# Optimization experiments

Hardware: AMD Instinct MI355X
Metric: run time of the kernel (lower is better)

Reference implementation:

```python
import jax, jax.numpy as jnp
import numpy as np
import math

D_MODEL = 1024
N_HEAD = 16
D_K = D_MODEL // N_HEAD
B, S = 2, 2048


def setup_inputs() -> dict:
    key = jax.random.key(0)
    ks = jax.random.split(key, 9)
    sc = 0.02
    return {
        "x": jax.random.normal(ks[0], (B, S, D_MODEL), dtype=jnp.float32),
        "Wq": jax.random.normal(ks[1], (D_MODEL, D_MODEL), dtype=jnp.float32) * sc,
        "bq": jnp.zeros((D_MODEL,), dtype=jnp.float32),
        "Wk": jax.random.normal(ks[2], (D_MODEL, D_MODEL), dtype=jnp.float32) * sc,
        "bk": jnp.zeros((D_MODEL,), dtype=jnp.float32),
        "Wv": jax.random.normal(ks[3], (D_MODEL, D_MODEL), dtype=jnp.float32) * sc,
        "bv": jnp.zeros((D_MODEL,), dtype=jnp.float32),
        "Wo": jax.random.normal(ks[4], (D_MODEL, D_MODEL), dtype=jnp.float32) * sc,
        "bo": jnp.zeros((D_MODEL,), dtype=jnp.float32),
    }


def reference(x, Wq, bq, Wk, bk, Wv, bv, Wo, bo):
    # cache=None prefill path: q_start=0, k_len=S (S <= MAX_CACHE_LEN)
    b, s, d = x.shape
    # projections (torch Linear: x @ W.T + b)
    q = (x @ Wq.T + bq).reshape(b, s, N_HEAD, D_K).transpose(0, 2, 1, 3)  # [b,h,s,dk]
    k = (x @ Wk.T + bk).reshape(b, s, N_HEAD, D_K).transpose(0, 2, 1, 3)
    v = (x @ Wv.T + bv).reshape(b, s, N_HEAD, D_K).transpose(0, 2, 1, 3)
    scores = jnp.einsum("bhqd,bhkd->bhqk", q, k) / math.sqrt(D_K)
    causal = jnp.triu(jnp.ones((s, s), dtype=bool), k=1)  # True above diagonal
    scores = jnp.where(causal[None, None], -jnp.inf, scores)
    attn = jax.nn.softmax(scores, axis=-1)  # dropout p=0 (eval)
    ctx = jnp.einsum("bhqk,bhkd->bhqd", attn, v)
    ctx = ctx.transpose(0, 2, 1, 3).reshape(b, s, d)
    return ctx @ Wo.T + bo
```

## Files before the change

### kernel.cpp

```cpp
#include <hip/hip_runtime.h>
#include <hip/hip_bf16.h>

#define DM 1024
#define NH 16
#define DK 64
#define BB 2
#define SS 2048
#define NTOK (BB*SS)
#define SCALE_LOG2E 0.1803368801111204f

typedef __attribute__((ext_vector_type(8))) short bf16x8;
typedef __attribute__((ext_vector_type(4))) float f32x4;
typedef __attribute__((ext_vector_type(4))) unsigned short us4;
typedef __attribute__((ext_vector_type(4))) unsigned int u32x4;

#define GLOAD16(gp, lp) \
  __builtin_amdgcn_global_load_lds((const __attribute__((address_space(1))) void*)(gp), \
                                   (__attribute__((address_space(3))) void*)(lp), 16, 0, 0)

__device__ inline unsigned short f2b(float f) {
  unsigned int x = __float_as_uint(f);
  return (unsigned short)((x + 0x7FFFu + ((x >> 16) & 1u)) >> 16);
}
__device__ inline unsigned int pack2bf(float a, float b) {
  unsigned int r;
  asm("v_cvt_pk_bf16_f32 %0, %1, %2" : "=v"(r) : "v"(a), "v"(b));
  return r;
}

#define XC4 (NTOK*DM/4)
#define WC4 (DM*DM/4)
__global__ void cast_all(const float* __restrict__ x,  const float* __restrict__ wq,
                         const float* __restrict__ wk, const float* __restrict__ wv,
                         const float* __restrict__ wo,
                         unsigned short* __restrict__ xb,  unsigned short* __restrict__ wqb,
                         unsigned short* __restrict__ wkb, unsigned short* __restrict__ wvb,
                         unsigned short* __restrict__ wob) {
  const int total = XC4 + 4*WC4;
  int i = blockIdx.x * blockDim.x + threadIdx.x;
  int stride = gridDim.x * blockDim.x;
  for (; i < total; i += stride) {
    const float* s; unsigned short* d; int off;
    if (i < XC4) { s = x; d = xb; off = i; }
    else {
      int j = i - XC4;
      int sel = j >> 18;
      off = j & (WC4 - 1);
      if      (sel == 0) { s = wq; d = wqb; }
      else if (sel == 1) { s = wk; d = wkb; }
      else if (sel == 2) { s = wv; d = wvb; }
      else               { s = wo; d = wob; }
    }
    float4 v = reinterpret_cast<const float4*>(s)[off];
    us4 o;
    o[0] = f2b(v.x); o[1] = f2b(v.y); o[2] = f2b(v.z); o[3] = f2b(v.w);
    reinterpret_cast<us4*>(d)[off] = o;
  }
}

__device__ __forceinline__ void gemm_mainloop(const unsigned short* __restrict__ A,
                                              const unsigned short* __restrict__ W,
                                              unsigned short* As, unsigned short* Bs,
                                              int m0, int n0, int tid, f32x4 acc[4][2]) {
  const int lane = tid & 63;
  const int w = tid >> 6;
  const int wr = w >> 1, wc = w & 1;
  const int g = lane >> 4, q = lane & 15;

  const int col0 = (((lane & 7) ^ ((lane >> 3) & 7)) << 3);
  const unsigned short* Ag = A + (size_t)(m0 + w*32 + (lane >> 3)) * DM + col0;
  const unsigned short* Bg = W + (size_t)(n0 + w*16 + (lane >> 3)) * DM + col0;
  char* AsB = (char*)As + w * 4096;
  char* BsB = (char*)Bs + w * 2048;

  const int fso = ((g ^ (q & 7)) << 4);

  for (int kt = 0; kt < DM; kt += 64) {
    __syncthreads();
    GLOAD16(Ag + kt,          AsB);
    GLOAD16(Ag + kt +  8*DM,  AsB + 1024);
    GLOAD16(Ag + kt + 16*DM,  AsB + 2048);
    GLOAD16(Ag + kt + 24*DM,  AsB + 3072);
    GLOAD16(Bg + kt,          BsB);
    GLOAD16(Bg + kt +  8*DM,  BsB + 1024);
    __syncthreads();
    #pragma unroll
    for (int h = 0; h < 2; h++) {
      const int so = fso ^ (h << 6);
      bf16x8 aF[4], bF[2];
      #pragma unroll
      for (int mt = 0; mt < 4; mt++)
        aF[mt] = *reinterpret_cast<const bf16x8*>((char*)As + (wr*64 + mt*16 + q)*128 + so);
      #pragma unroll
      for (int nt = 0; nt < 2; nt++)
        bF[nt] = *reinterpret_cast<const bf16x8*>((char*)Bs + (wc*32 + nt*16 + q)*128 + so);
      #pragma unroll
      for (int mt = 0; mt < 4; mt++)
        #pragma unroll
        for (int nt = 0; nt < 2; nt++)
          acc[mt][nt] = __builtin_amdgcn_mfma_f32_16x16x32_bf16(aF[mt], bF[nt], acc[mt][nt], 0, 0, 0);
    }
  }
}

__global__ __launch_bounds__(256, 2)
void gemm_qkv(const unsigned short* __restrict__ xb,
              const unsigned short* __restrict__ wqb, const unsigned short* __restrict__ wkb,
              const unsigned short* __restrict__ wvb,
              const float* __restrict__ bq, const float* __restrict__ bk,
              const float* __restrict__ bv,
              unsigned short* __restrict__ qo, unsigned short* __restrict__ ko,
              unsigned short* __restrict__ vto) {
  __shared__ unsigned short As[128*64];
  __shared__ unsigned short Bs[64*64];
  const int z = blockIdx.z;
  const unsigned short* W = (z == 0) ? wqb : (z == 1) ? wkb : wvb;
  const float* bias = (z == 0) ? bq : (z == 1) ? bk : bv;
  const int m0 = blockIdx.y * 128, n0 = blockIdx.x * 64;

  f32x4 acc[4][2];
  #pragma unroll
  for (int i = 0; i < 4; i++)
    #pragma unroll
    for (int j = 0; j < 2; j++)
      #pragma unroll
      for (int e = 0; e < 4; e++) acc[i][j][e] = 0.f;

  gemm_mainloop(xb, W, As, Bs, m0, n0, threadIdx.x, acc);

  const int lane = threadIdx.x & 63, w = threadIdx.x >> 6;
  const int wr = w >> 1, wc = w & 1, g = lane >> 4, q = lane & 15;
  const float sc = (z == 0) ? SCALE_LOG2E : 1.0f;
  #pragma unroll
  for (int mt = 0; mt < 4; mt++) {
    #pragma unroll
    for (int nt = 0; nt < 2; nt++) {
      const int mg0 = m0 + wr*64 + mt*16 + 4*g;
      const int ng  = n0 + wc*32 + nt*16 + q;
      const float bv_ = bias[ng];
      const int h = ng >> 6, d = ng & 63;
      if (z == 2) {
        const int b = mg0 >> 11, s = mg0 & 2047;
        us4 pk;
        #pragma unroll
        for (int r = 0; r < 4; r++) pk[r] = f2b(acc[mt][nt][r] + bv_);
        *reinterpret_cast<us4*>(&vto[((size_t)((b*NH + h)*DK + d)) * SS + s]) = pk;
      } else {
        unsigned short* out = (z == 0) ? qo : ko;
        #pragma unroll
        for (int r = 0; r < 4; r++) {
          const int m = mg0 + r;
          const int b = m >> 11, s = m & 2047;
          out[((size_t)((b*NH + h)*SS + s)) * DK + d] = f2b((acc[mt][nt][r] + bv_) * sc);
        }
      }
    }
  }
}

__global__ __launch_bounds__(256, 2)
void gemm_out(const unsigned short* __restrict__ ctx,
              const unsigned short* __restrict__ wob,
              const float* __restrict__ bo, float* __restrict__ out) {
  __shared__ unsigned short As[128*64];
  __shared__ unsigned short Bs[64*64];
  const int m0 = blockIdx.y * 128, n0 = blockIdx.x * 64;
  f32x4 acc[4][2];
  #pragma unroll
  for (int i = 0; i < 4; i++)
    #pragma unroll
    for (int j = 0; j < 2; j++)
      #pragma unroll
      for (int e = 0; e < 4; e++) acc[i][j][e] = 0.f;

  gemm_mainloop(ctx, wob, As, Bs, m0, n0, threadIdx.x, acc);

  const int lane = threadIdx.x & 63, w = threadIdx.x >> 6;
  const int wr = w >> 1, wc = w & 1, g = lane >> 4, q = lane & 15;
  #pragma unroll
  for (int mt = 0; mt < 4; mt++) {
    #pragma unroll
    for (int nt = 0; nt < 2; nt++) {
      const int mg0 = m0 + wr*64 + mt*16 + 4*g;
      const int ng  = n0 + wc*32 + nt*16 + q;
      const float bv_ = bo[ng];
      #pragma unroll
      for (int r = 0; r < 4; r++)
        out[(size_t)(mg0 + r) * DM + ng] = acc[mt][nt][r] + bv_;
    }
  }
}

__global__ __launch_bounds__(256, 2)
void attn_fwd(const unsigned short* __restrict__ Q,
              const unsigned short* __restrict__ Kg,
              const unsigned short* __restrict__ VT,
              unsigned short* __restrict__ ctx) {
  __shared__ float CMB[2][64][66];
  __shared__ float CML[2][64];
  const int qblk = (int)gridDim.y - 1 - (int)blockIdx.y;
  const int bh = blockIdx.x;
  const int tid = threadIdx.x;
  const int lane = tid & 63;
  const int w = tid >> 6;
  const int g = lane >> 4;
  const int q = lane & 15;
  const int q0 = qblk * 64;
  const int T = qblk + 1;
  const size_t base = (size_t)bh * SS * DK;

  bf16x8 aQ[4][2];
  #pragma unroll
  for (int rg = 0; rg < 4; rg++) {
    const unsigned short* qp = Q + base + (size_t)(q0 + rg*16 + q) * DK + g*8;
    aQ[rg][0] = *reinterpret_cast<const bf16x8*>(qp);
    aQ[rg][1] = *reinterpret_cast<const bf16x8*>(qp + 32);
  }

  f32x4 o[4][4];
  float l_run[4];
  #pragma unroll
  for (int rg = 0; rg < 4; rg++) {
    #pragma unroll
    for (int dt = 0; dt < 4; dt++)
      #pragma unroll
      for (int r = 0; r < 4; r++) o[rg][dt][r] = 0.f;
    l_run[rg] = 0.f;
  }

  const int src0 = q + 32*(g & 1);
  const int src1 = src0 + 16;
  const bool gsel = (g >> 1);

  bf16x8 aK[4][2], aV[4][2];
  if (w < T) {
    #pragma unroll
    for (int f = 0; f < 4; f++) {
      const unsigned short* kp = Kg + base + (size_t)(w*64 + f*16 + q) * DK + g*8;
      aK[f][0] = *reinterpret_cast<const bf16x8*>(kp);
      aK[f][1] = *reinterpret_cast<const bf16x8*>(kp + 32);
    }
    #pragma unroll
    for (int dt = 0; dt < 4; dt++) {
      const unsigned short* vp = VT + base + (size_t)(dt*16 + q) * SS + w*64 + g*8;
      aV[dt][0] = *reinterpret_cast<const bf16x8*>(vp);
      aV[dt][1] = *reinterpret_cast<const bf16x8*>(vp + 32);
    }
  }

  for (int t = w; t < T; t += 4) {
    const bool tail = (t == T - 1);
    #pragma unroll
    for (int rg = 0; rg < 4; rg++) {
      f32x4 sf[4];
      __builtin_amdgcn_s_setprio(1);
      #pragma unroll
      for (int f = 0; f < 4; f++) {
        f32x4 z;
        #pragma unroll
        for (int r = 0; r < 4; r++) z[r] = 0.f;
        z = __builtin_amdgcn_mfma_f32_16x16x32_bf16(aK[f][0], aQ[rg][0], z, 0, 0, 0);
        z = __builtin_amdgcn_mfma_f32_16x16x32_bf16(aK[f][1], aQ[rg][1], z, 0, 0, 0);
        sf[f] = z;
      }
      __builtin_amdgcn_s_setprio(0);

      if (rg == 3 && t + 4 < T) {
        #pragma unroll
        for (int f = 0; f < 4; f++) {
          const unsigned short* kp = Kg + base + (size_t)((t+4)*64 + f*16 + q) * DK + g*8;
          aK[f][0] = *reinterpret_cast<const bf16x8*>(kp);
          aK[f][1] = *reinterpret_cast<const bf16x8*>(kp + 32);
        }
      }

      const int grow = q0 + rg*16 + q;
      float p[4][4];
      float ps = 0.f;
      #pragma unroll
      for (int f = 0; f < 4; f++)
        #pragma unroll
        for (int r = 0; r < 4; r++) {
          float v = sf[f][r];
          if (tail) {
            int gcol = t*64 + f*16 + 4*g + r;
            if (gcol > grow) v = -1e30f;
          }
          float e = exp2f(v);
          p[f][r] = e;
          ps += e;
        }
      ps += __shfl_xor(ps, 16);
      ps += __shfl_xor(ps, 32);
      l_run[rg] += ps;

      unsigned int pk[4][2];
      #pragma unroll
      for (int f = 0; f < 4; f++) {
        pk[f][0] = pack2bf(p[f][0], p[f][1]);
        pk[f][1] = pack2bf(p[f][2], p[f][3]);
      }

      u32x4 bl, bh2;
      #pragma unroll
      for (int t2 = 0; t2 < 4; t2++) {
        const int src = (t2 < 2) ? src0 : src1;
        unsigned int s0 = (unsigned int)__shfl((int)pk[0][t2 & 1], src);
        unsigned int s1 = (unsigned int)__shfl((int)pk[1][t2 & 1], src);
        unsigned int s2 = (unsigned int)__shfl((int)pk[2][t2 & 1], src);
        unsigned int s3 = (unsigned int)__shfl((int)pk[3][t2 & 1], src);
        bl[t2]  = gsel ? s1 : s0;
        bh2[t2] = gsel ? s3 : s2;
      }
      bf16x8 Blo = __builtin_bit_cast(bf16x8, bl);
      bf16x8 Bhi = __builtin_bit_cast(bf16x8, bh2);

      __builtin_amdgcn_s_setprio(1);
      #pragma unroll
      for (int dt = 0; dt < 4; dt++) {
        o[rg][dt] = __builtin_amdgcn_mfma_f32_16x16x32_bf16(aV[dt][0], Blo, o[rg][dt], 0, 0, 0);
        o[rg][dt] = __builtin_amdgcn_mfma_f32_16x16x32_bf16(aV[dt][1], Bhi, o[rg][dt], 0, 0, 0);
      }
      __builtin_amdgcn_s_setprio(0);
    }

    if (t + 4 < T) {
      #pragma unroll
      for (int dt = 0; dt < 4; dt++) {
        const unsigned short* vp = VT + base + (size_t)(dt*16 + q) * SS + (t+4)*64 + g*8;
        aV[dt][0] = *reinterpret_cast<const bf16x8*>(vp);
        aV[dt][1] = *reinterpret_cast<const bf16x8*>(vp + 32);
      }
    }
  }

  if (w >= 2) {
    const int slot = w - 2;
    #pragma unroll
    for (int rg = 0; rg < 4; rg++) {
      #pragma unroll
      for (int dt = 0; dt < 4; dt++)
        #pragma unroll
        for (int r = 0; r < 4; r++)
          CMB[slot][rg*16 + q][dt*16 + 4*g + r] = o[rg][dt][r];
      CML[slot][rg*16 + q] = l_run[rg];
    }
  }
  __syncthreads();
  if (w < 2) {
    const int slot = w;
    #pragma unroll
    for (int rg = 0; rg < 4; rg++) {
      l_run[rg] += CML[slot][rg*16 + q];
      #pragma unroll
      for (int dt = 0; dt < 4; dt++)
        #pragma unroll
        for (int r = 0; r < 4; r++)
          o[rg][dt][r] += CMB[slot][rg*16 + q][dt*16 + 4*g + r];
    }
  }
  __syncthreads();
  if (w == 1) {
    #pragma unroll
    for (int rg = 0; rg < 4; rg++) {
      #pragma unroll
      for (int dt = 0; dt < 4; dt++)
        #pragma unroll
        for (int r = 0; r < 4; r++)
          CMB[0][rg*16 + q][dt*16 + 4*g + r] = o[rg][dt][r];
      CML[0][rg*16 + q] = l_run[rg];
    }
  }
  __syncthreads();
  if (w == 0) {
    const int b = bh >> 4, h = bh & 15;
    #pragma unroll
    for (int rg = 0; rg < 4; rg++) {
      float lfin = l_run[rg] + CML[0][rg*16 + q];
      const float inv = 1.0f / lfin;
      const int s = q0 + rg*16 + q;
      #pragma unroll
      for (int dt = 0; dt < 4; dt++) {
        us4 pkv;
        #pragma unroll
        for (int r = 0; r < 4; r++) {
          float val = o[rg][dt][r] + CMB[0][rg*16 + q][dt*16 + 4*g + r];
          pkv[r] = f2b(val * inv);
        }
        *reinterpret_cast<us4*>(&ctx[((size_t)(b*SS + s)) * DM + h*DK + dt*16 + 4*g]) = pkv;
      }
    }
  }
}

extern "C" void kernel_launch(void* const* d_in, const int* in_sizes, int n_in,
                              void* d_out, int out_size, void* d_ws, size_t ws_size,
                              hipStream_t stream) {
  const float* x  = (const float*)d_in[0];
  const float* Wq = (const float*)d_in[1];
  const float* bq = (const float*)d_in[2];
  const float* Wk = (const float*)d_in[3];
  const float* bk = (const float*)d_in[4];
  const float* Wv = (const float*)d_in[5];
  const float* bv = (const float*)d_in[6];
  const float* Wo = (const float*)d_in[7];
  const float* bo = (const float*)d_in[8];
  float* out = (float*)d_out;

  unsigned short* xb  = (unsigned short*)d_ws;
  unsigned short* wqb = xb  + (size_t)NTOK * DM;
  unsigned short* wkb = wqb + (size_t)DM * DM;
  unsigned short* wvb = wkb + (size_t)DM * DM;
  unsigned short* wob = wvb + (size_t)DM * DM;
  unsigned short* q   = wob + (size_t)DM * DM;
  unsigned short* k   = q   + (size_t)NTOK * DM;
  unsigned short* vt  = k   + (size_t)NTOK * DM;
  unsigned short* ctx = vt  + (size_t)NTOK * DM;

  cast_all<<<2048, 256, 0, stream>>>(x, Wq, Wk, Wv, Wo, xb, wqb, wkb, wvb, wob);

  gemm_qkv<<<dim3(DM/64, NTOK/128, 3), 256, 0, stream>>>(xb, wqb, wkb, wvb,
                                                         bq, bk, bv, q, k, vt);

  attn_fwd<<<dim3(BB*NH, SS/64), 256, 0, stream>>>(q, k, vt, ctx);

  gemm_out<<<dim3(DM/64, NTOK/128), 256, 0, stream>>>(ctx, wob, bo, out);
}
```

Measured before the change: 116.1 us.

## Pair causal query blocks per workgroup and use 16x16x16 MFMA for PV

Each attention workgroup now handles two query blocks, pairing block i with block 31-i, so every block does equal causal work and the grid shrinks from 32 to 16 along y. The PV product switches from 16x16x32 MFMAs fed by cross-lane shuffles to 16x16x16 MFMAs, which consume the softmax probabilities directly in their accumulator layout; V is loaded in 4-element chunks to match. This removes the shuffle permutation and the load imbalance of the causal triangle. In exchange it issues twice as many MFMA instructions, each half the size, runs the two blocks serially inside one workgroup, adds an extra barrier between them, and halves the number of workgroups available to fill the GPU.

```diff
diff --git a/kernel.cpp b/kernel.cpp
--- a/kernel.cpp
+++ b/kernel.cpp
@@ -10,9 +10,9 @@
 #define SCALE_LOG2E 0.1803368801111204f
 
 typedef __attribute__((ext_vector_type(8))) short bf16x8;
+typedef __attribute__((ext_vector_type(4))) short s16x4;
 typedef __attribute__((ext_vector_type(4))) float f32x4;
 typedef __attribute__((ext_vector_type(4))) unsigned short us4;
-typedef __attribute__((ext_vector_type(4))) unsigned int u32x4;
 
 #define GLOAD16(gp, lp) \
   __builtin_amdgcn_global_load_lds((const __attribute__((address_space(1))) void*)(gp), \
@@ -26,6 +26,16 @@
   unsigned int r;
   asm("v_cvt_pk_bf16_f32 %0, %1, %2" : "=v"(r) : "v"(a), "v"(b));
   return r;
+}
+
+__device__ inline f32x4 mfma16(s16x4 a, s16x4 b, f32x4 c) {
+#if __has_builtin(__builtin_amdgcn_mfma_f32_16x16x16bf16_1k)
+  return __builtin_amdgcn_mfma_f32_16x16x16bf16_1k(a, b, c, 0, 0, 0);
+#else
+  f32x4 d;
+  asm("v_mfma_f32_16x16x16_bf16 %0, %1, %2, %3" : "=v"(d) : "v"(a), "v"(b), "v"(c));
+  return d;
+#endif
 }
 
 #define XC4 (NTOK*DM/4)
@@ -198,196 +208,188 @@
               unsigned short* __restrict__ ctx) {
   __shared__ float CMB[2][64][66];
   __shared__ float CML[2][64];
-  const int qblk = (int)gridDim.y - 1 - (int)blockIdx.y;
+  const int pairIdx = blockIdx.y;
   const int bh = blockIdx.x;
   const int tid = threadIdx.x;
   const int lane = tid & 63;
   const int w = tid >> 6;
   const int g = lane >> 4;
   const int q = lane & 15;
-  const int q0 = qblk * 64;
-  const int T = qblk + 1;
   const size_t base = (size_t)bh * SS * DK;
-
-  bf16x8 aQ[4][2];
-  #pragma unroll
-  for (int rg = 0; rg < 4; rg++) {
-    const unsigned short* qp = Q + base + (size_t)(q0 + rg*16 + q) * DK + g*8;
-    aQ[rg][0] = *reinterpret_cast<const bf16x8*>(qp);
-    aQ[rg][1] = *reinterpret_cast<const bf16x8*>(qp + 32);
-  }
-
-  f32x4 o[4][4];
-  float l_run[4];
-  #pragma unroll
-  for (int rg = 0; rg < 4; rg++) {
-    #pragma unroll
-    for (int dt = 0; dt < 4; dt++)
-      #pragma unroll
-      for (int r = 0; r < 4; r++) o[rg][dt][r] = 0.f;
-    l_run[rg] = 0.f;
-  }
-
-  const int src0 = q + 32*(g & 1);
-  const int src1 = src0 + 16;
-  const bool gsel = (g >> 1);
-
-  bf16x8 aK[4][2], aV[4][2];
-  if (w < T) {
-    #pragma unroll
-    for (int f = 0; f < 4; f++) {
-      const unsigned short* kp = Kg + base + (size_t)(w*64 + f*16 + q) * DK + g*8;
-      aK[f][0] = *reinterpret_cast<const bf16x8*>(kp);
-      aK[f][1] = *reinterpret_cast<const bf16x8*>(kp + 32);
-    }
-    #pragma unroll
-    for (int dt = 0; dt < 4; dt++) {
-      const unsigned short* vp = VT + base + (size_t)(dt*16 + q) * SS + w*64 + g*8;
-      aV[dt][0] = *reinterpret_cast<const bf16x8*>(vp);
-      aV[dt][1] = *reinterpret_cast<const bf16x8*>(vp + 32);
-    }
-  }
-
-  for (int t = w; t < T; t += 4) {
-    const bool tail = (t == T - 1);
+  const int b = bh >> 4, h = bh & 15;
+
+  for (int grp = 0; grp < 2; grp++) {
+    const int qblk = grp ? (31 - pairIdx) : pairIdx;
+    const int q0 = qblk * 64;
+    const int T = qblk + 1;
+
+    bf16x8 aQ[4][2];
     #pragma unroll
     for (int rg = 0; rg < 4; rg++) {
-      f32x4 sf[4];
-      __builtin_amdgcn_s_setprio(1);
+      const unsigned short* qp = Q + base + (size_t)(q0 + rg*16 + q) * DK + g*8;
+      aQ[rg][0] = *reinterpret_cast<const bf16x8*>(qp);
+      aQ[rg][1] = *reinterpret_cast<const bf16x8*>(qp + 32);
+    }
+
+    f32x4 o[4][4];
+    float l_run[4];
+    #pragma unroll
+    for (int rg = 0; rg < 4; rg++) {
+      #pragma unroll
+      for (int dt = 0; dt < 4; dt++)
+        #pragma unroll
+        for (int r = 0; r < 4; r++) o[rg][dt][r] = 0.f;
+      l_run[rg] = 0.f;
+    }
+
+    bf16x8 aK[4][2];
+    s16x4 aV16[4][4];
+    if (w < T) {
       #pragma unroll
       for (int f = 0; f < 4; f++) {
-        f32x4 z;
-        #pragma unroll
-        for (int r = 0; r < 4; r++) z[r] = 0.f;
-        z = __builtin_amdgcn_mfma_f32_16x16x32_bf16(aK[f][0], aQ[rg][0], z, 0, 0, 0);
-        z = __builtin_amdgcn_mfma_f32_16x16x32_bf16(aK[f][1], aQ[rg][1], z, 0, 0, 0);
-        sf[f] = z;
-      }
-      __builtin_amdgcn_s_setprio(0);
-
-      if (rg == 3 && t + 4 < T) {
+        const unsigned short* kp = Kg + base + (size_t)(w*64 + f*16 + q) * DK + g*8;
+        aK[f][0] = *reinterpret_cast<const bf16x8*>(kp);
+        aK[f][1] = *reinterpret_cast<const bf16x8*>(kp + 32);
+      }
+      #pragma unroll
+      for (int dt = 0; dt < 4; dt++)
+        #pragma unroll
+        for (int f = 0; f < 4; f++)
+          aV16[dt][f] = *reinterpret_cast<const s16x4*>(
+              VT + base + (size_t)(dt*16 + q) * SS + w*64 + f*16 + 4*g);
+    }
+
+    for (int t = w; t < T; t += 4) {
+      const bool tail = (t == T - 1);
+      #pragma unroll
+      for (int rg = 0; rg < 4; rg++) {
+        f32x4 sf[4];
+        __builtin_amdgcn_s_setprio(1);
         #pragma unroll
         for (int f = 0; f < 4; f++) {
-          const unsigned short* kp = Kg + base + (size_t)((t+4)*64 + f*16 + q) * DK + g*8;
-          aK[f][0] = *reinterpret_cast<const bf16x8*>(kp);
-          aK[f][1] = *reinterpret_cast<const bf16x8*>(kp + 32);
+          f32x4 z;
+          #pragma unroll
+          for (int r = 0; r < 4; r++) z[r] = 0.f;
+          z = __builtin_amdgcn_mfma_f32_16x16x32_bf16(aK[f][0], aQ[rg][0], z, 0, 0, 0);
+          z = __builtin_amdgcn_mfma_f32_16x16x32_bf16(aK[f][1], aQ[rg][1], z, 0, 0, 0);
+          sf[f] = z;
         }
-      }
-
-      const int grow = q0 + rg*16 + q;
-      float p[4][4];
-      float ps = 0.f;
-      #pragma unroll
-      for (int f = 0; f < 4; f++)
-        #pragma unroll
-        for (int r = 0; r < 4; r++) {
-          float v = sf[f][r];
-          if (tail) {
-            int gcol = t*64 + f*16 + 4*g + r;
-            if (gcol > grow) v = -1e30f;
+        __builtin_amdgcn_s_setprio(0);
+
+        if (rg == 3 && t + 4 < T) {
+          #pragma unroll
+          for (int f = 0; f < 4; f++) {
+            const unsigned short* kp = Kg + base + (size_t)((t+4)*64 + f*16 + q) * DK + g*8;
+            aK[f][0] = *reinterpret_cast<const bf16x8*>(kp);
+            aK[f][1] = *reinterpret_cast<const bf16x8*>(kp + 32);
           }
-          float e = exp2f(v);
-          p[f][r] = e;
-          ps += e;
         }
-      ps += __shfl_xor(ps, 16);
-      ps += __shfl_xor(ps, 32);
-      l_run[rg] += ps;
-
-      unsigned int pk[4][2];
-      #pragma unroll
-      for (int f = 0; f < 4; f++) {
-        pk[f][0] = pack2bf(p[f][0], p[f][1]);
-        pk[f][1] = pack2bf(p[f][2], p[f][3]);
-      }
-
-      u32x4 bl, bh2;
-      #pragma unroll
-      for (int t2 = 0; t2 < 4; t2++) {
-        const int src = (t2 < 2) ? src0 : src1;
-        unsigned int s0 = (unsigned int)__shfl((int)pk[0][t2 & 1], src);
-        unsigned int s1 = (unsigned int)__shfl((int)pk[1][t2 & 1], src);
-        unsigned int s2 = (unsigned int)__shfl((int)pk[2][t2 & 1], src);
-        unsigned int s3 = (unsigned int)__shfl((int)pk[3][t2 & 1], src);
-        bl[t2]  = gsel ? s1 : s0;
-        bh2[t2] = gsel ? s3 : s2;
-      }
-      bf16x8 Blo = __builtin_bit_cast(bf16x8, bl);
-      bf16x8 Bhi = __builtin_bit_cast(bf16x8, bh2);
-
-      __builtin_amdgcn_s_setprio(1);
-      #pragma unroll
-      for (int dt = 0; dt < 4; dt++) {
-        o[rg][dt] = __builtin_amdgcn_mfma_f32_16x16x32_bf16(aV[dt][0], Blo, o[rg][dt], 0, 0, 0);
-        o[rg][dt] = __builtin_amdgcn_mfma_f32_16x16x32_bf16(aV[dt][1], Bhi, o[rg][dt], 0, 0, 0);
-      }
-      __builtin_amdgcn_s_setprio(0);
-    }
-
-    if (t + 4 < T) {
-      #pragma unroll
-      for (int dt = 0; dt < 4; dt++) {
-        const unsigned short* vp = VT + base + (size_t)(dt*16 + q) * SS + (t+4)*64 + g*8;
-        aV[dt][0] = *reinterpret_cast<const bf16x8*>(vp);
-        aV[dt][1] = *reinterpret_cast<const bf16x8*>(vp + 32);
-      }
-    }
-  }
-
-  if (w >= 2) {
-    const int slot = w - 2;
-    #pragma unroll
-    for (int rg = 0; rg < 4; rg++) {
-      #pragma unroll
-      for (int dt = 0; dt < 4; dt++)
-        #pragma unroll
-        for (int r = 0; r < 4; r++)
-          CMB[slot][rg*16 + q][dt*16 + 4*g + r] = o[rg][dt][r];
-      CML[slot][rg*16 + q] = l_run[rg];
-    }
-  }
-  __syncthreads();
-  if (w < 2) {
-    const int slot = w;
-    #pragma unroll
-    for (int rg = 0; rg < 4; rg++) {
-      l_run[rg] += CML[slot][rg*16 + q];
-      #pragma unroll
-      for (int dt = 0; dt < 4; dt++)
-        #pragma unroll
-        for (int r = 0; r < 4; r++)
-          o[rg][dt][r] += CMB[slot][rg*16 + q][dt*16 + 4*g + r];
-    }
-  }
-  __syncthreads();
-  if (w == 1) {
-    #pragma unroll
-    for (int rg = 0; rg < 4; rg++) {
-      #pragma unroll
-      for (int dt = 0; dt < 4; dt++)
-        #pragma unroll
-        for (int r = 0; r < 4; r++)
-          CMB[0][rg*16 + q][dt*16 + 4*g + r] = o[rg][dt][r];
-      CML[0][rg*16 + q] = l_run[rg];
-    }
-  }
-  __syncthreads();
-  if (w == 0) {
-    const int b = bh >> 4, h = bh & 15;
-    #pragma unroll
-    for (int rg = 0; rg < 4; rg++) {
-      float lfin = l_run[rg] + CML[0][rg*16 + q];
-      const float inv = 1.0f / lfin;
-      const int s = q0 + rg*16 + q;
-      #pragma unroll
-      for (int dt = 0; dt < 4; dt++) {
-        us4 pkv;
-        #pragma unroll
-        for (int r = 0; r < 4; r++) {
-          float val = o[rg][dt][r] + CMB[0][rg*16 + q][dt*16 + 4*g + r];
-          pkv[r] = f2b(val * inv);
+
+        const int grow = q0 + rg*16 + q;
+        float p[4][4];
+        float ps = 0.f;
+        #pragma unroll
+        for (int f = 0; f < 4; f++)
+          #pragma unroll
+          for (int r = 0; r < 4; r++) {
+            float v = sf[f][r];
+            if (tail) {
+              int gcol = t*64 + f*16 + 4*g + r;
+              if (gcol > grow) v = -1e30f;
+            }
+            float e = exp2f(v);
+            p[f][r] = e;
+            ps += e;
+          }
+        ps += __shfl_xor(ps, 16);
+        ps += __shfl_xor(ps, 32);
+        l_run[rg] += ps;
+
+        s16x4 pb[4];
+        #pragma unroll
+        for (int f = 0; f < 4; f++) {
+          unsigned int lo = pack2bf(p[f][0], p[f][1]);
+          unsigned int hi = pack2bf(p[f][2], p[f][3]);
+          pb[f][0] = (short)(lo & 0xFFFF);
+          pb[f][1] = (short)(lo >> 16);
+          pb[f][2] = (short)(hi & 0xFFFF);
+          pb[f][3] = (short)(hi >> 16);
         }
-        *reinterpret_cast<us4*>(&ctx[((size_t)(b*SS + s)) * DM + h*DK + dt*16 + 4*g]) = pkv;
+
+        __builtin_amdgcn_s_setprio(1);
+        #pragma unroll
+        for (int f = 0; f < 4; f++)
+          #pragma unroll
+          for (int dt = 0; dt < 4; dt++)
+            o[rg][dt] = mfma16(aV16[dt][f], pb[f], o[rg][dt]);
+        __builtin_amdgcn_s_setprio(0);
+      }
+
+      if (t + 4 < T) {
+        #pragma unroll
+        for (int dt = 0; dt < 4; dt++)
+          #pragma unroll
+          for (int f = 0; f < 4; f++)
+            aV16[dt][f] = *reinterpret_cast<const s16x4*>(
+                VT + base + (size_t)(dt*16 + q) * SS + (t+4)*64 + f*16 + 4*g);
+      }
+    }
+
+    if (grp) __syncthreads();
+    if (w >= 2) {
+      const int slot = w - 2;
+      #pragma unroll
+      for (int rg = 0; rg < 4; rg++) {
+        #pragma unroll
+        for (int dt = 0; dt < 4; dt++)
+          #pragma unroll
+          for (int r = 0; r < 4; r++)
+            CMB[slot][rg*16 + q][dt*16 + 4*g + r] = o[rg][dt][r];
+        CML[slot][rg*16 + q] = l_run[rg];
+      }
+    }
+    __syncthreads();
+    if (w < 2) {
+      const int slot = w;
+      #pragma unroll
+      for (int rg = 0; rg < 4; rg++) {
+        l_run[rg] += CML[slot][rg*16 + q];
+        #pragma unroll
+        for (int dt = 0; dt < 4; dt++)
+          #pragma unroll
+          for (int r = 0; r < 4; r++)
+            o[rg][dt][r] += CMB[slot][rg*16 + q][dt*16 + 4*g + r];
+      }
+    }
+    __syncthreads();
+    if (w == 1) {
+      #pragma unroll
+      for (int rg = 0; rg < 4; rg++) {
+        #pragma unroll
+        for (int dt = 0; dt < 4; dt++)
+          #pragma unroll
+          for (int r = 0; r < 4; r++)
+            CMB[0][rg*16 + q][dt*16 + 4*g + r] = o[rg][dt][r];
+        CML[0][rg*16 + q] = l_run[rg];
+      }
+    }
+    __syncthreads();
+    if (w == 0) {
+      #pragma unroll
+      for (int rg = 0; rg < 4; rg++) {
+        float lfin = l_run[rg] + CML[0][rg*16 + q];
+        const float inv = 1.0f / lfin;
+        const int s = q0 + rg*16 + q;
+        #pragma unroll
+        for (int dt = 0; dt < 4; dt++) {
+          us4 pkv;
+          #pragma unroll
+          for (int r = 0; r < 4; r++) {
+            float val = o[rg][dt][r] + CMB[0][rg*16 + q][dt*16 + 4*g + r];
+            pkv[r] = f2b(val * inv);
+          }
+          *reinterpret_cast<us4*>(&ctx[((size_t)(b*SS + s)) * DM + h*DK + dt*16 + 4*g]) = pkv;
+        }
       }
     }
   }
@@ -422,7 +424,7 @@
   gemm_qkv<<<dim3(DM/64, NTOK/128, 3), 256, 0, stream>>>(xb, wqb, wkb, wvb,
                                                          bq, bk, bv, q, k, vt);
 
-  attn_fwd<<<dim3(BB*NH, SS/64), 256, 0, stream>>>(q, k, vt, ctx);
+  attn_fwd<<<dim3(BB*NH, 16), 256, 0, stream>>>(q, k, vt, ctx);
 
   gemm_out<<<dim3(DM/64, NTOK/128), 256, 0, stream>>>(ctx, wob, bo, out);
 }
```

After: 134.8 us. 16.1% more time.
